# Optimization experiments

Measured on AMD Instinct MI355X. Metric: run time of the kernel, lower is better.

## Reference

```python
import jax, jax.numpy as jnp
import numpy as np

# conv hyperparams matching init_kwargs (kernel=3, stride=1, pad=1, dilation=1, dg=1)
KH = KW = 3
SH = SW = 1
PH = PW = 1
DH = DW = 1


def setup_inputs() -> dict:
    key = jax.random.key(0)
    k1, k2, k3 = jax.random.split(key, 3)
    N, C, H, W = 4, 64, 128, 128
    OC, KN = 64, KH * KW
    x = jax.random.normal(k1, (N, C, H, W), jnp.float32)
    # offset channels: deformable_groups * kernel_n * 2, ordered (y, x) per point
    offset = jax.random.normal(k2, (N, KN * 2, H, W), jnp.float32)
    weight = jax.random.normal(k3, (OC, C, KN), jnp.float32) * 0.05
    return {"x": x, "offset": offset, "weight": weight}


def _bilinear(img, ix, iy):
    # img: (C, H, W); ix, iy: (KN, OH, OW) pixel coords; align_corners=True, zeros padding
    H, W = img.shape[1], img.shape[2]
    x0 = jnp.floor(ix)
    y0 = jnp.floor(iy)
    x1 = x0 + 1.0
    y1 = y0 + 1.0
    wx1 = ix - x0
    wx0 = 1.0 - wx1
    wy1 = iy - y0
    wy0 = 1.0 - wy1

    def gather(xc, yc, w):
        xi = jnp.clip(xc, 0, W - 1).astype(jnp.int32)
        yi = jnp.clip(yc, 0, H - 1).astype(jnp.int32)
        m = ((xc >= 0) & (xc <= W - 1) & (yc >= 0) & (yc <= H - 1)).astype(img.dtype)
        return img[:, yi, xi] * (w * m)[None]  # (C, KN, OH, OW)

    return (gather(x0, y0, wx0 * wy0) + gather(x1, y0, wx1 * wy0)
            + gather(x0, y1, wx0 * wy1) + gather(x1, y1, wx1 * wy1))


def reference(x, offset, weight):
    N, C, H, W = x.shape
    KN = weight.shape[2]
    OH, OW = offset.shape[2], offset.shape[3]
    half_h = (H - 1) / 2.0
    half_w = (W - 1) / 2.0
    # base mesh in normalized [-1,1] coords (same for every kernel point, per source)
    ys = jnp.arange(OH, dtype=x.dtype) * SH - PH + ((KH - 1) // 2) * DH
    xs = jnp.arange(OW, dtype=x.dtype) * SW - PW + ((KW - 1) // 2) * DW
    base_gy = (ys - half_h) / half_h  # (OH,)
    base_gx = (xs - half_w) / half_w  # (OW,)
    off = offset.reshape(N, KN, 2, OH, OW)
    gy = base_gy[None, None, :, None] + off[:, :, 0] / half_h  # (N, KN, OH, OW)
    gx = base_gx[None, None, None, :] + off[:, :, 1] / half_w
    # back to pixel coords (align_corners=True)
    ix = (gx + 1.0) * half_w
    iy = (gy + 1.0) * half_h
    sampled = jax.vmap(_bilinear)(x, ix, iy)  # (N, C, KN, OH, OW)
    # weight (OC, C, KN) contracted over (C, KN); note: source forward never adds bias
    out = jnp.einsum('oik,nikhw->nohw', weight, sampled)
    return out
```

## Files before the change

### kernel.cpp

```cpp
#include <hip/hip_runtime.h>
#include <hip/hip_bf16.h>


#define NB 4
#define CI 64
#define HH 128
#define WW 128
#define OCH 64
#define KNN 9
#define HW (HH * WW)

typedef unsigned int u32;
typedef unsigned short u16;
typedef __attribute__((ext_vector_type(8))) short bf16x8;
typedef __attribute__((ext_vector_type(4))) float f32x4;

__device__ inline u16 f2bf(float f) {
    u32 u = __float_as_uint(f);
    return (u16)((u + 0x7fffu + ((u >> 16) & 1u)) >> 16);
}
__device__ inline u32 pk2(float lo, float hi) {
    return (u32)f2bf(lo) | ((u32)f2bf(hi) << 16);
}
__device__ inline void up2(u32 u, float& lo, float& hi) {
    lo = __uint_as_float(u << 16);
    hi = __uint_as_float(u & 0xffff0000u);
}

__global__ __launch_bounds__(256) void prep_kernel(const float* __restrict__ x,
                                                   const float* __restrict__ w,
                                                   u16* __restrict__ xT,
                                                   u16* __restrict__ wf) {
    __shared__ float T[64 * 68];
    const int tid = threadIdx.x;
    if (blockIdx.x < NB * 256) {
        const int n = blockIdx.x >> 8;
        const int hw0 = (blockIdx.x & 255) << 6;
#pragma unroll
        for (int jj = 0; jj < 4; jj++) {
            int c = (tid >> 4) + (jj << 4);
            int hwq = (tid & 15) << 2;
            float4 v = *(const float4*)&x[(((n << 6) + c) << 14) + hw0 + hwq];
            *(float4*)&T[c * 68 + hwq] = v;
        }
        __syncthreads();
        const int hw_l = tid >> 2;
        const int cb = (tid & 3) << 4;
        u32 ou[8];
#pragma unroll
        for (int k = 0; k < 8; k++) {
            ou[k] = pk2(T[(cb + 2 * k) * 68 + hw_l], T[(cb + 2 * k + 1) * 68 + hw_l]);
        }
        u16* dst = xT + ((size_t)((n << 14) + hw0 + hw_l) << 6) + cb;
        *(uint4*)dst = make_uint4(ou[0], ou[1], ou[2], ou[3]);
        *(uint4*)(dst + 8) = make_uint4(ou[4], ou[5], ou[6], ou[7]);
    } else {
        int i = (blockIdx.x - NB * 256) * 256 + tid;
        if (i < KNN * 2 * 4 * 64 * 8) {
            int j = i & 7, l = (i >> 3) & 63, strip = (i >> 9) & 3,
                chunk = (i >> 11) & 1, kn = i >> 12;
            int oc = strip * 16 + (l & 15);
            int c = chunk * 32 + ((l >> 4) & 3) * 8 + j;
            wf[i] = f2bf(w[(oc * CI + c) * KNN + kn]);
        }
    }
}

__global__ __launch_bounds__(256, 3) void dcn_main_kernel(const u16* __restrict__ xT,
                                                          const float* __restrict__ off,
                                                          const u16* __restrict__ wf,
                                                          float* __restrict__ out) {
    __shared__ __align__(16) u16 tile[256 * 72];
    const int tid = threadIdx.x;
    const int l = tid & 63;
    const int wv = tid >> 6;

    const int b = blockIdx.x;
    const int xcd = b & 7;
    const int n = xcd >> 1;
    const int patch = (b >> 3) + ((xcd & 1) << 7);
    const int py = ((patch >> 4) << 3), px = ((patch & 15) << 3);
    const int ty = min(max(py - 4, 0), HH - 16);
    const int tx = min(max(px - 4, 0), WW - 16);

    const u16* xTn = xT + ((size_t)n << 20);
    const float* offn = off + n * (2 * KNN * HW);

    {
        const int tr = tid >> 4, tc = tid & 15;
        const u16* src = xTn + ((((ty + tr) << 7) + (tx + tc)) << 6);
        u16* dst = &tile[tid * 72];
#pragma unroll
        for (int j = 0; j < 8; j++) {
            *(uint4*)(dst + j * 8) = *(const uint4*)(src + j * 8);
        }
    }

    const int qy = ((wv >> 1) << 2), qx = ((wv & 1) << 2);
    const int col = l & 15;
    const int oh = py + qy + (col >> 2);
    const int ow = px + qx + (col & 3);
    const int rr = (oh << 7) + ow;
    const int cbase = (l >> 4) << 3;

    float offy[KNN], offx[KNN];
#pragma unroll
    for (int kn = 0; kn < KNN; kn++) {
        offy[kn] = offn[(2 * kn) * HW + rr];
        offx[kn] = offn[(2 * kn + 1) * HW + rr];
    }

    __syncthreads();

    const bf16x8* wfv = (const bf16x8*)wf;
    f32x4 acc[4] = {{0, 0, 0, 0}, {0, 0, 0, 0}, {0, 0, 0, 0}, {0, 0, 0, 0}};

#pragma unroll
    for (int kn = 0; kn < KNN; kn++) {
        float iy = (float)oh + offy[kn], ix = (float)ow + offx[kn];
        float y0f = floorf(iy), x0f = floorf(ix);
        float wy1 = iy - y0f, wy0 = 1.f - wy1;
        float wx1 = ix - x0f, wx0 = 1.f - wx1;
        float my0 = (y0f >= 0.f && y0f <= 127.f) ? 1.f : 0.f;
        float my1 = (y0f >= -1.f && y0f <= 126.f) ? 1.f : 0.f;
        float mx0 = (x0f >= 0.f && x0f <= 127.f) ? 1.f : 0.f;
        float mx1 = (x0f >= -1.f && x0f <= 126.f) ? 1.f : 0.f;
        float W0 = wy0 * wx0 * my0 * mx0, W1 = wy0 * wx1 * my0 * mx1;
        float W2 = wy1 * wx0 * my1 * mx0, W3 = wy1 * wx1 * my1 * mx1;
        int y0 = min(max((int)y0f, 0), 127), y1 = min(max((int)y0f + 1, 0), 127);
        int x0 = min(max((int)x0f, 0), 127), x1 = min(max((int)x0f + 1, 0), 127);

        const int dy0 = min(max(y0 - ty, 0), 15), dy1 = min(max(y1 - ty, 0), 15);
        const int dx0 = min(max(x0 - tx, 0), 15), dx1 = min(max(x1 - tx, 0), 15);
        const int p00 = (dy0 << 4) + dx0, p01 = (dy0 << 4) + dx1;
        const int p10 = (dy1 << 4) + dx0, p11 = (dy1 << 4) + dx1;
        const bool oot = (y0 < ty) | (y1 > ty + 15) | (x0 < tx) | (x1 > tx + 15);

        uint4 q[8];
        q[0] = *(const uint4*)&tile[p00 * 72 + cbase];
        q[1] = *(const uint4*)&tile[p01 * 72 + cbase];
        q[2] = *(const uint4*)&tile[p10 * 72 + cbase];
        q[3] = *(const uint4*)&tile[p11 * 72 + cbase];
        q[4] = *(const uint4*)&tile[p00 * 72 + cbase + 32];
        q[5] = *(const uint4*)&tile[p01 * 72 + cbase + 32];
        q[6] = *(const uint4*)&tile[p10 * 72 + cbase + 32];
        q[7] = *(const uint4*)&tile[p11 * 72 + cbase + 32];
        if (oot) {
            const int O0 = ((y0 << 7) + x0) << 6, O1 = ((y0 << 7) + x1) << 6;
            const int O2 = ((y1 << 7) + x0) << 6, O3 = ((y1 << 7) + x1) << 6;
            q[0] = *(const uint4*)(xTn + O0 + cbase);
            q[1] = *(const uint4*)(xTn + O1 + cbase);
            q[2] = *(const uint4*)(xTn + O2 + cbase);
            q[3] = *(const uint4*)(xTn + O3 + cbase);
            q[4] = *(const uint4*)(xTn + O0 + cbase + 32);
            q[5] = *(const uint4*)(xTn + O1 + cbase + 32);
            q[6] = *(const uint4*)(xTn + O2 + cbase + 32);
            q[7] = *(const uint4*)(xTn + O3 + cbase + 32);
        }

#pragma unroll
        for (int ch = 0; ch < 2; ch++) {
            const u32* a0 = (const u32*)&q[ch * 4 + 0];
            const u32* a1 = (const u32*)&q[ch * 4 + 1];
            const u32* a2 = (const u32*)&q[ch * 4 + 2];
            const u32* a3 = (const u32*)&q[ch * 4 + 3];
            union { u32 u[4]; bf16x8 v; } B;
#pragma unroll
            for (int k = 0; k < 4; k++) {
                float p0l, p0h, p1l, p1h, p2l, p2h, p3l, p3h;
                up2(a0[k], p0l, p0h);
                up2(a1[k], p1l, p1h);
                up2(a2[k], p2l, p2h);
                up2(a3[k], p3l, p3h);
                float slo = p0l * W0 + p1l * W1 + p2l * W2 + p3l * W3;
                float shi = p0h * W0 + p1h * W1 + p2h * W2 + p3h * W3;
                B.u[k] = pk2(slo, shi);
            }
#pragma unroll
            for (int s = 0; s < 4; s++) {
                bf16x8 A = wfv[((((kn << 1) + ch) << 2) + s) * 64 + l];
                acc[s] = __builtin_amdgcn_mfma_f32_16x16x32_bf16(A, B.v, acc[s], 0, 0, 0);
            }
        }
    }

    const int rq = l >> 4;
    float* op = out + ((size_t)(n * OCH) << 14);
#pragma unroll
    for (int s = 0; s < 4; s++) {
        const int ocb = (s << 4) + (rq << 2);
#pragma unroll
        for (int g = 0; g < 4; g++) {
            op[((ocb + g) << 14) + rr] = acc[s][g];
        }
    }
}

__global__ __launch_bounds__(256) void dcn_fallback_kernel(
    const float* __restrict__ x, const float* __restrict__ off,
    const float* __restrict__ w, float* __restrict__ out) {
    int p = blockIdx.x * blockDim.x + threadIdx.x;
    int n = p / HW, r = p % HW, oh = r / WW, ow = r % WW;
    float acc[OCH];
#pragma unroll
    for (int i = 0; i < OCH; i++) acc[i] = 0.f;
    const float* xn = x + n * (CI * HW);
    const float* offn = off + n * (2 * KNN * HW);
    for (int kn = 0; kn < KNN; kn++) {
        float iy = (float)oh + offn[(2 * kn) * HW + r];
        float ix = (float)ow + offn[(2 * kn + 1) * HW + r];
        float y0f = floorf(iy), x0f = floorf(ix);
        float wy1 = iy - y0f, wy0 = 1.f - wy1, wx1 = ix - x0f, wx0 = 1.f - wx1;
        float my0 = (y0f >= 0.f && y0f <= 127.f) ? 1.f : 0.f;
        float my1 = (y0f >= -1.f && y0f <= 126.f) ? 1.f : 0.f;
        float mx0 = (x0f >= 0.f && x0f <= 127.f) ? 1.f : 0.f;
        float mx1 = (x0f >= -1.f && x0f <= 126.f) ? 1.f : 0.f;
        float w00 = wy0 * wx0 * my0 * mx0, w01 = wy0 * wx1 * my0 * mx1;
        float w10 = wy1 * wx0 * my1 * mx0, w11 = wy1 * wx1 * my1 * mx1;
        int y0 = min(max((int)y0f, 0), 127), y1 = min(max((int)y0f + 1, 0), 127);
        int x0 = min(max((int)x0f, 0), 127), x1 = min(max((int)x0f + 1, 0), 127);
        int o00 = y0 * WW + x0, o01 = y0 * WW + x1, o10 = y1 * WW + x0, o11 = y1 * WW + x1;
        for (int c = 0; c < CI; c++) {
            const float* xc = xn + c * HW;
            float s = xc[o00] * w00 + xc[o01] * w01 + xc[o10] * w10 + xc[o11] * w11;
#pragma unroll
            for (int oc = 0; oc < OCH; oc++) acc[oc] += w[(oc * CI + c) * KNN + kn] * s;
        }
    }
    float* outp = out + n * (OCH * HW) + r;
#pragma unroll
    for (int oc = 0; oc < OCH; oc++) outp[oc * HW] = acc[oc];
}

extern "C" void kernel_launch(void* const* d_in, const int* in_sizes, int n_in,
                              void* d_out, int out_size, void* d_ws, size_t ws_size,
                              hipStream_t stream) {
    const float* x = (const float*)d_in[0];
    const float* off = (const float*)d_in[1];
    const float* w = (const float*)d_in[2];
    float* out = (float*)d_out;

    const size_t xT_elems = (size_t)NB * HW * CI;
    const size_t wf_elems = (size_t)KNN * 2 * 4 * 64 * 8;
    const size_t need = (xT_elems + wf_elems) * sizeof(u16);

    if (ws_size >= need) {
        u16* xT = (u16*)d_ws;
        u16* wfr = xT + xT_elems;
        const int wf_blocks = (int)((wf_elems + 255) / 256);
        prep_kernel<<<NB * 256 + wf_blocks, 256, 0, stream>>>(x, w, xT, wfr);
        dcn_main_kernel<<<NB * 256, 256, 0, stream>>>(xT, off, wfr, out);
    } else {
        dcn_fallback_kernel<<<(NB * HW) / 256, 256, 0, stream>>>(x, off, w, out);
    }
}
```

Measured before the change: 102.3 us.

## Shrink LDS tile to 14x16 with stride 68 to raise occupancy to four blocks

Result: no change. 101.5 us (-0.8%).

```diff
diff --git a/kernel.cpp b/kernel.cpp
--- a/kernel.cpp
+++ b/kernel.cpp
@@ -9,6 +9,7 @@
 #define OCH 64
 #define KNN 9
 #define HW (HH * WW)
+#define TSTR 68
 
 typedef unsigned int u32;
 typedef unsigned short u16;
@@ -22,9 +23,13 @@
 __device__ inline u32 pk2(float lo, float hi) {
     return (u32)f2bf(lo) | ((u32)f2bf(hi) << 16);
 }
-__device__ inline void up2(u32 u, float& lo, float& hi) {
-    lo = __uint_as_float(u << 16);
-    hi = __uint_as_float(u & 0xffff0000u);
+__device__ inline float2 up2v(u32 u) {
+    return float2{__uint_as_float(u << 16), __uint_as_float(u & 0xffff0000u)};
+}
+__device__ inline u32 pkrn(float2 s) {
+    union { __hip_bfloat162 b; u32 u; } c;
+    c.b = __float22bfloat162_rn(s);
+    return c.u;
 }
 
 __global__ __launch_bounds__(256) void prep_kernel(const float* __restrict__ x,
@@ -66,11 +71,11 @@
     }
 }
 
-__global__ __launch_bounds__(256, 3) void dcn_main_kernel(const u16* __restrict__ xT,
+__global__ __launch_bounds__(256, 4) void dcn_main_kernel(const u16* __restrict__ xT,
                                                           const float* __restrict__ off,
                                                           const u16* __restrict__ wf,
                                                           float* __restrict__ out) {
-    __shared__ __align__(16) u16 tile[256 * 72];
+    __shared__ __align__(16) u16 tile[224 * TSTR];
     const int tid = threadIdx.x;
     const int l = tid & 63;
     const int wv = tid >> 6;
@@ -80,19 +85,19 @@
     const int n = xcd >> 1;
     const int patch = (b >> 3) + ((xcd & 1) << 7);
     const int py = ((patch >> 4) << 3), px = ((patch & 15) << 3);
-    const int ty = min(max(py - 4, 0), HH - 16);
+    const int ty = min(max(py - 3, 0), HH - 14);
     const int tx = min(max(px - 4, 0), WW - 16);
 
     const u16* xTn = xT + ((size_t)n << 20);
     const float* offn = off + n * (2 * KNN * HW);
 
-    {
+    if (tid < 224) {
         const int tr = tid >> 4, tc = tid & 15;
         const u16* src = xTn + ((((ty + tr) << 7) + (tx + tc)) << 6);
-        u16* dst = &tile[tid * 72];
-#pragma unroll
-        for (int j = 0; j < 8; j++) {
-            *(uint4*)(dst + j * 8) = *(const uint4*)(src + j * 8);
+        u16* dst = &tile[tid * TSTR];
+#pragma unroll
+        for (int j = 0; j < 16; j++) {
+            *(uint2*)(dst + j * 4) = *(const uint2*)(src + j * 4);
         }
     }
 
@@ -101,7 +106,7 @@
     const int oh = py + qy + (col >> 2);
     const int ow = px + qx + (col & 3);
     const int rr = (oh << 7) + ow;
-    const int cbase = (l >> 4) << 3;
+    const int cb = (l >> 4) << 3;
 
     float offy[KNN], offx[KNN];
 #pragma unroll
@@ -130,56 +135,72 @@
         int y0 = min(max((int)y0f, 0), 127), y1 = min(max((int)y0f + 1, 0), 127);
         int x0 = min(max((int)x0f, 0), 127), x1 = min(max((int)x0f + 1, 0), 127);
 
-        const int dy0 = min(max(y0 - ty, 0), 15), dy1 = min(max(y1 - ty, 0), 15);
+        const int dy0 = min(max(y0 - ty, 0), 13), dy1 = min(max(y1 - ty, 0), 13);
         const int dx0 = min(max(x0 - tx, 0), 15), dx1 = min(max(x1 - tx, 0), 15);
         const int p00 = (dy0 << 4) + dx0, p01 = (dy0 << 4) + dx1;
         const int p10 = (dy1 << 4) + dx0, p11 = (dy1 << 4) + dx1;
-        const bool oot = (y0 < ty) | (y1 > ty + 15) | (x0 < tx) | (x1 > tx + 15);
-
-        uint4 q[8];
-        q[0] = *(const uint4*)&tile[p00 * 72 + cbase];
-        q[1] = *(const uint4*)&tile[p01 * 72 + cbase];
-        q[2] = *(const uint4*)&tile[p10 * 72 + cbase];
-        q[3] = *(const uint4*)&tile[p11 * 72 + cbase];
-        q[4] = *(const uint4*)&tile[p00 * 72 + cbase + 32];
-        q[5] = *(const uint4*)&tile[p01 * 72 + cbase + 32];
-        q[6] = *(const uint4*)&tile[p10 * 72 + cbase + 32];
-        q[7] = *(const uint4*)&tile[p11 * 72 + cbase + 32];
+        const bool oot = (y0 < ty) | (y1 > ty + 13) | (x0 < tx) | (x1 > tx + 15);
+
+        uint2 q[16];
+#pragma unroll
+        for (int cc = 0; cc < 2; cc++) {
+            const int o = cb + (cc << 5);
+            q[cc * 8 + 0] = *(const uint2*)&tile[p00 * TSTR + o];
+            q[cc * 8 + 1] = *(const uint2*)&tile[p00 * TSTR + o + 4];
+            q[cc * 8 + 2] = *(const uint2*)&tile[p01 * TSTR + o];
+            q[cc * 8 + 3] = *(const uint2*)&tile[p01 * TSTR + o + 4];
+            q[cc * 8 + 4] = *(const uint2*)&tile[p10 * TSTR + o];
+            q[cc * 8 + 5] = *(const uint2*)&tile[p10 * TSTR + o + 4];
+            q[cc * 8 + 6] = *(const uint2*)&tile[p11 * TSTR + o];
+            q[cc * 8 + 7] = *(const uint2*)&tile[p11 * TSTR + o + 4];
+        }
         if (oot) {
             const int O0 = ((y0 << 7) + x0) << 6, O1 = ((y0 << 7) + x1) << 6;
             const int O2 = ((y1 << 7) + x0) << 6, O3 = ((y1 << 7) + x1) << 6;
-            q[0] = *(const uint4*)(xTn + O0 + cbase);
-            q[1] = *(const uint4*)(xTn + O1 + cbase);
-            q[2] = *(const uint4*)(xTn + O2 + cbase);
-            q[3] = *(const uint4*)(xTn + O3 + cbase);
-            q[4] = *(const uint4*)(xTn + O0 + cbase + 32);
-            q[5] = *(const uint4*)(xTn + O1 + cbase + 32);
-            q[6] = *(const uint4*)(xTn + O2 + cbase + 32);
-            q[7] = *(const uint4*)(xTn + O3 + cbase + 32);
-        }
-
-#pragma unroll
-        for (int ch = 0; ch < 2; ch++) {
-            const u32* a0 = (const u32*)&q[ch * 4 + 0];
-            const u32* a1 = (const u32*)&q[ch * 4 + 1];
-            const u32* a2 = (const u32*)&q[ch * 4 + 2];
-            const u32* a3 = (const u32*)&q[ch * 4 + 3];
+#pragma unroll
+            for (int cc = 0; cc < 2; cc++) {
+                const int o = cb + (cc << 5);
+                q[cc * 8 + 0] = *(const uint2*)(xTn + O0 + o);
+                q[cc * 8 + 1] = *(const uint2*)(xTn + O0 + o + 4);
+                q[cc * 8 + 2] = *(const uint2*)(xTn + O1 + o);
+                q[cc * 8 + 3] = *(const uint2*)(xTn + O1 + o + 4);
+                q[cc * 8 + 4] = *(const uint2*)(xTn + O2 + o);
+                q[cc * 8 + 5] = *(const uint2*)(xTn + O2 + o + 4);
+                q[cc * 8 + 6] = *(const uint2*)(xTn + O3 + o);
+                q[cc * 8 + 7] = *(const uint2*)(xTn + O3 + o + 4);
+            }
+        }
+
+#pragma unroll
+        for (int cc = 0; cc < 2; cc++) {
             union { u32 u[4]; bf16x8 v; } B;
 #pragma unroll
             for (int k = 0; k < 4; k++) {
-                float p0l, p0h, p1l, p1h, p2l, p2h, p3l, p3h;
-                up2(a0[k], p0l, p0h);
-                up2(a1[k], p1l, p1h);
-                up2(a2[k], p2l, p2h);
-                up2(a3[k], p3l, p3h);
-                float slo = p0l * W0 + p1l * W1 + p2l * W2 + p3l * W3;
-                float shi = p0h * W0 + p1h * W1 + p2h * W2 + p3h * W3;
-                B.u[k] = pk2(slo, shi);
-            }
-#pragma unroll
-            for (int s = 0; s < 4; s++) {
-                bf16x8 A = wfv[((((kn << 1) + ch) << 2) + s) * 64 + l];
-                acc[s] = __builtin_amdgcn_mfma_f32_16x16x32_bf16(A, B.v, acc[s], 0, 0, 0);
+                const int hi = k & 1;
+                u32 d0 = hi ? q[cc * 8 + 1].y : (k >> 1) ? q[cc * 8 + 1].x
+                                                         : (hi ? q[cc * 8 + 0].y : q[cc * 8 + 0].x);
+                (void)d0;
+            }
+            u32 c0d[4] = {q[cc * 8 + 0].x, q[cc * 8 + 0].y, q[cc * 8 + 1].x, q[cc * 8 + 1].y};
+            u32 c1d[4] = {q[cc * 8 + 2].x, q[cc * 8 + 2].y, q[cc * 8 + 3].x, q[cc * 8 + 3].y};
+            u32 c2d[4] = {q[cc * 8 + 4].x, q[cc * 8 + 4].y, q[cc * 8 + 5].x, q[cc * 8 + 5].y};
+            u32 c3d[4] = {q[cc * 8 + 6].x, q[cc * 8 + 6].y, q[cc * 8 + 7].x, q[cc * 8 + 7].y};
+#pragma unroll
+            for (int k = 0; k < 4; k++) {
+                float2 s = up2v(c0d[k]);
+                s.x *= W0; s.y *= W0;
+                float2 c1 = up2v(c1d[k]);
+                s.x = fmaf(c1.x, W1, s.x); s.y = fmaf(c1.y, W1, s.y);
+                float2 c2 = up2v(c2d[k]);
+                s.x = fmaf(c2.x, W2, s.x); s.y = fmaf(c2.y, W2, s.y);
+                float2 c3 = up2v(c3d[k]);
+                s.x = fmaf(c3.x, W3, s.x); s.y = fmaf(c3.y, W3, s.y);
+                B.u[k] = pkrn(s);
+            }
+#pragma unroll
+            for (int s4 = 0; s4 < 4; s4++) {
+                bf16x8 A = wfv[((((kn << 1) + cc) << 2) + s4) * 64 + l];
+                acc[s4] = __builtin_amdgcn_mfma_f32_16x16x32_bf16(A, B.v, acc[s4], 0, 0, 0);
             }
         }
     }
```
